# Performance work log

Hardware: AMD Instinct MI355X
Metric: run time of the kernel (lower is better)

Reference implementation:

```python
import jax, jax.numpy as jnp
import numpy as np

B = 16384          # batch
F = 26             # num sparse features
D = 13             # num dense features
V = 100000         # vocab per sparse feature
E = 16             # embedding size
HID = [400, 400, 400]
DNN_IN = F * E + D  # 429


def setup_inputs() -> dict:
    key = jax.random.key(0)
    ks = jax.random.split(key, 16)
    inp = {}
    inp["x_sparse"] = jax.random.randint(ks[0], (B, F), 0, V, dtype=jnp.int32)
    inp["x_dense"] = jax.random.uniform(ks[1], (B, D), dtype=jnp.float32)
    # embedding tables (stacked across features; all vocabs equal)
    inp["emb1"] = jax.random.normal(ks[2], (F, V, 1), dtype=jnp.float32) * 0.0001
    inp["emb2"] = jax.random.normal(ks[3], (F, V, E), dtype=jnp.float32) * 0.0001
    inp["w_dense"] = jax.random.normal(ks[4], (D, 1), dtype=jnp.float32) * 0.0001
    inp["bias"] = jnp.zeros((1,), dtype=jnp.float32)
    dims = [DNN_IN] + HID
    for i in range(3):
        inp[f"dnn_w{i}"] = jax.random.normal(ks[5 + i], (dims[i], dims[i + 1]), dtype=jnp.float32) * 0.02
        inp[f"dnn_b{i}"] = jnp.zeros((dims[i + 1],), dtype=jnp.float32)
    inp["final_w"] = jax.random.normal(ks[9], (HID[-1], 1), dtype=jnp.float32) * 0.02
    return inp


def reference(x_sparse, x_dense, emb1, emb2, w_dense, bias,
              dnn_w0, dnn_b0, dnn_w1, dnn_b1, dnn_w2, dnn_b2, final_w):
    f_idx = jnp.arange(F)[None, :]                      # [1, F]
    # FM linear: per-feature 1-d embedding lookup, summed over features
    e1 = emb1[f_idx, x_sparse, 0]                       # [B, F]
    linear_sparse = jnp.sum(e1, axis=-1, keepdims=True)  # [B, 1]
    linear_dense = x_dense @ w_dense                    # [B, 1]
    logit = linear_sparse + linear_dense
    # FM second order: square-of-sum minus sum-of-square
    fm = emb2[f_idx, x_sparse]                          # [B, F, E]
    s = jnp.sum(fm, axis=1)                             # [B, E]
    cross = 0.5 * jnp.sum(s * s - jnp.sum(fm * fm, axis=1), axis=-1, keepdims=True)  # [B, 1]
    logit = logit + cross
    # DNN
    h = jnp.concatenate([fm.reshape(x_sparse.shape[0], F * E), x_dense], axis=-1)  # [B, F*E+D]
    h = jax.nn.relu(h @ dnn_w0 + dnn_b0)
    h = jax.nn.relu(h @ dnn_w1 + dnn_b1)
    h = jax.nn.relu(h @ dnn_w2 + dnn_b2)
    logit = logit + h @ final_w                         # [B, 1]
    return jax.nn.sigmoid(logit + bias)
```

## Files before the change

### kernel.cpp

```cpp
#include <hip/hip_runtime.h>
#include <hip/hip_bf16.h>
#include <math.h>

#define BATCH 16384
#define NF 26
#define ND 13
#define VOC 100000
#define KP0 448
#define KP1 416
#define CS 112
#define NSL 4
#define NGB 4096
#define NPB 2240

typedef __bf16 bf16x8 __attribute__((ext_vector_type(8)));
typedef float f32x4 __attribute__((ext_vector_type(4)));
using bf16 = __hip_bfloat16;
typedef unsigned short u16;

__device__ __forceinline__ void gload_lds16(const void* g, void* l) {
  __builtin_amdgcn_global_load_lds(
      (const __attribute__((address_space(1))) void*)g,
      (__attribute__((address_space(3))) void*)l, 16, 0, 0);
}

__device__ __forceinline__ u16 f2bu(float v) {
  union { __hip_bfloat16 b; u16 u; } cv;
  cv.b = __float2bfloat16(v);
  return cv.u;
}

__global__ __launch_bounds__(256) void prep_gather_kernel(
    const float* __restrict__ w0, const float* __restrict__ w1,
    const float* __restrict__ w2, bf16* __restrict__ wt0,
    bf16* __restrict__ wt1, bf16* __restrict__ wt2,
    const int* __restrict__ xs, const float* __restrict__ xd,
    const float* __restrict__ emb1, const float* __restrict__ emb2,
    const float* __restrict__ wd, const float* __restrict__ biasp,
    bf16* __restrict__ h0, float* __restrict__ partial) {
  const int bid = blockIdx.x, tid = threadIdx.x;
  if (bid >= NGB) {
    const int pbid = bid - NGB;
    const float* W; bf16* Wt; int K, KP, idx;
    if (pbid < 784)       { W = w0; Wt = wt0; K = 429; KP = KP0; idx = pbid * 256 + tid; }
    else if (pbid < 1512) { W = w1; Wt = wt1; K = 400; KP = KP1; idx = (pbid - 784) * 256 + tid; }
    else                  { W = w2; Wt = wt2; K = 400; KP = KP1; idx = (pbid - 1512) * 256 + tid; }
    int k = idx % KP, n = idx / KP;
    float v = (k < K && n < 400) ? W[(size_t)k * 400 + n] : 0.f;
    Wt[idx] = __float2bfloat16(v);
    return;
  }
  const int p = bid;
  const int x8 = p & 7, qb = p >> 3;
  const int gl = (qb >> 5) * 256 + x8 * 32 + (qb & 31);
  const int w = tid >> 6, lane = tid & 63;
  const int b = gl * 4 + w;
  const int q = lane >> 2, sub = lane & 3;

  int xsl = 0;
  if (lane < NF) xsl = xs[b * NF + lane];
  float lin = 0.f;
  if (lane < NF) lin = emb1[(size_t)lane * VOC + xsl];
  if (lane < ND) lin += xd[b * ND + lane] * wd[lane];

  float4 sv = make_float4(0.f, 0.f, 0.f, 0.f);
  float sq = 0.f;
#pragma unroll
  for (int i = 0; i < 2; ++i) {
    int f = i * 16 + q;
    if (f < NF) {
      int idx = __shfl(xsl, f);
      float4 v = *((const float4*)(emb2 + ((size_t)f * VOC + idx) * 16) + sub);
      sv.x += v.x; sv.y += v.y; sv.z += v.z; sv.w += v.w;
      sq += v.x * v.x + v.y * v.y + v.z * v.z + v.w * v.w;
      ushort4 st;
      st.x = f2bu(v.x); st.y = f2bu(v.y); st.z = f2bu(v.z); st.w = f2bu(v.w);
      *(ushort4*)(h0 + (size_t)b * KP0 + f * 16 + sub * 4) = st;
    }
  }
  if (lane < 32) {
    float v = (lane < ND) ? xd[b * ND + lane] : 0.f;
    h0[(size_t)b * KP0 + 416 + lane] = __float2bfloat16(v);
  }
#pragma unroll
  for (int off = 4; off < 64; off <<= 1) {
    sv.x += __shfl_xor(sv.x, off);
    sv.y += __shfl_xor(sv.y, off);
    sv.z += __shfl_xor(sv.z, off);
    sv.w += __shfl_xor(sv.w, off);
  }
  float t = sv.x * sv.x + sv.y * sv.y + sv.z * sv.z + sv.w * sv.w;
#pragma unroll
  for (int off = 1; off < 64; off <<= 1) {
    t += __shfl_xor(t, off);
    sq += __shfl_xor(sq, off);
    lin += __shfl_xor(lin, off);
  }
  if (lane == 0)
    partial[b] = biasp[0] + lin + 0.5f * (t * 0.0625f - sq);
}

template <int NK, bool FINAL>
__global__ __launch_bounds__(256, 2) void gemm_kernel(
    const bf16* __restrict__ A, const bf16* __restrict__ Wt,
    const float* __restrict__ bias, bf16* __restrict__ outH,
    const float* __restrict__ fw, float* __restrict__ dotb) {
  constexpr int KP = NK * 32;
  constexpr int NKB = NK - 7;
  extern __shared__ __align__(16) char smem[];
  const int b = blockIdx.x, tid = threadIdx.x;
  const int w = tid >> 6, lane = tid & 63, r = lane & 15, g = lane >> 4;
  const int lane8 = b & 7, hi = b >> 3;
  const int s = hi & 3, mchunk = (hi >> 2) * 8 + lane8;
  const int row0 = mchunk * 128, col0 = s * CS;
  const char* wbase = (const char*)(Wt + (size_t)col0 * KP);

  auto stageP = [&](int kbase, int chunks) {
    for (int c0 = 0; c0 < chunks; c0 += 256) {
      int c = c0 + tid;
      if (c < chunks) {
        int kk = c / (CS * 4);
        int rm = c - kk * (CS * 4);
        int n = rm >> 2, j = rm & 3;
        int kc = j ^ ((n >> 1) & 3);
        gload_lds16(wbase + (size_t)n * (KP * 2) + (kbase + kk) * 64 + kc * 16,
                    smem + (c0 + w * 64) * 16);
      }
    }
  };

  const char* Ab = (const char*)(A + (size_t)(row0 + w * 32 + r) * KP) + g * 16;
  const size_t rtS = (size_t)16 * KP * 2;

  bf16x8 aA0[7], aA1[7];
#pragma unroll
  for (int k = 0; k < 7; ++k) {
    aA0[k] = *(const bf16x8*)(Ab + k * 64);
    aA1[k] = *(const bf16x8*)(Ab + k * 64 + rtS);
  }
  stageP(0, 7 * CS * 4);
  __syncthreads();

  bf16x8 aB0[NKB], aB1[NKB];
#pragma unroll
  for (int k = 0; k < NKB; ++k) {
    aB0[k] = *(const bf16x8*)(Ab + (7 + k) * 64);
    aB1[k] = *(const bf16x8*)(Ab + (7 + k) * 64 + rtS);
  }

  f32x4 acc[2][7];
#pragma unroll
  for (int rt = 0; rt < 2; ++rt)
#pragma unroll
    for (int ct = 0; ct < 7; ++ct) acc[rt][ct] = (f32x4){0.f, 0.f, 0.f, 0.f};

  const int swz = ((g ^ ((r >> 1) & 3)) << 4);
#pragma unroll
  for (int kk = 0; kk < 7; ++kk) {
    const char* sb = smem + kk * (CS * 64) + r * 64 + swz;
#pragma unroll
    for (int ct = 0; ct < 7; ++ct) {
      bf16x8 bfr = *(const bf16x8*)(sb + ct * 1024);
      acc[0][ct] = __builtin_amdgcn_mfma_f32_16x16x32_bf16(aA0[kk], bfr, acc[0][ct], 0, 0, 0);
      acc[1][ct] = __builtin_amdgcn_mfma_f32_16x16x32_bf16(aA1[kk], bfr, acc[1][ct], 0, 0, 0);
    }
  }
  __syncthreads();
  stageP(7, NKB * CS * 4);
  __syncthreads();
#pragma unroll
  for (int kk = 0; kk < NKB; ++kk) {
    const char* sb = smem + kk * (CS * 64) + r * 64 + swz;
#pragma unroll
    for (int ct = 0; ct < 7; ++ct) {
      bf16x8 bfr = *(const bf16x8*)(sb + ct * 1024);
      acc[0][ct] = __builtin_amdgcn_mfma_f32_16x16x32_bf16(aB0[kk], bfr, acc[0][ct], 0, 0, 0);
      acc[1][ct] = __builtin_amdgcn_mfma_f32_16x16x32_bf16(aB1[kk], bfr, acc[1][ct], 0, 0, 0);
    }
  }

  if (!FINAL) {
#pragma unroll
    for (int ct = 0; ct < 7; ++ct) {
      int col = col0 + ct * 16 + r;
      if (col < 400) {
        float bv = bias[col];
#pragma unroll
        for (int rt = 0; rt < 2; ++rt)
#pragma unroll
          for (int q = 0; q < 4; ++q) {
            float v = fmaxf(acc[rt][ct][q] + bv, 0.f);
            outH[(size_t)(row0 + w * 32 + rt * 16 + g * 4 + q) * KP1 + col] =
                __float2bfloat16(v);
          }
      }
    }
  } else {
    float pr[2][4] = {{0.f, 0.f, 0.f, 0.f}, {0.f, 0.f, 0.f, 0.f}};
#pragma unroll
    for (int ct = 0; ct < 7; ++ct) {
      int col = col0 + ct * 16 + r;
      if (col < 400) {
        float bv = bias[col], fv = fw[col];
#pragma unroll
        for (int rt = 0; rt < 2; ++rt)
#pragma unroll
          for (int q = 0; q < 4; ++q)
            pr[rt][q] += fmaxf(acc[rt][ct][q] + bv, 0.f) * fv;
      }
    }
#pragma unroll
    for (int rt = 0; rt < 2; ++rt)
#pragma unroll
      for (int q = 0; q < 4; ++q) {
        pr[rt][q] += __shfl_xor(pr[rt][q], 1);
        pr[rt][q] += __shfl_xor(pr[rt][q], 2);
        pr[rt][q] += __shfl_xor(pr[rt][q], 4);
        pr[rt][q] += __shfl_xor(pr[rt][q], 8);
      }
    if (r < 4) {
#pragma unroll
      for (int rt = 0; rt < 2; ++rt) {
        float v = (r == 0) ? pr[rt][0] : (r == 1) ? pr[rt][1]
                : (r == 2) ? pr[rt][2] : pr[rt][3];
        dotb[(size_t)s * BATCH + row0 + w * 32 + rt * 16 + g * 4 + r] = v;
      }
    }
  }
}

__global__ void finish_kernel(const float* __restrict__ partial,
                              const float* __restrict__ dotb,
                              float* __restrict__ out) {
  int i = blockIdx.x * 256 + threadIdx.x;
  if (i < BATCH) {
    float x = partial[i] + dotb[i] + dotb[BATCH + i] + dotb[2 * BATCH + i]
            + dotb[3 * BATCH + i];
    out[i] = 1.f / (1.f + expf(-x));
  }
}

extern "C" void kernel_launch(void* const* d_in, const int* in_sizes, int n_in,
                              void* d_out, int out_size, void* d_ws, size_t ws_size,
                              hipStream_t stream) {
  const int* xs = (const int*)d_in[0];
  const float* xd = (const float*)d_in[1];
  const float* emb1 = (const float*)d_in[2];
  const float* emb2 = (const float*)d_in[3];
  const float* wd = (const float*)d_in[4];
  const float* bias = (const float*)d_in[5];
  const float* w0 = (const float*)d_in[6];
  const float* b0 = (const float*)d_in[7];
  const float* w1 = (const float*)d_in[8];
  const float* b1 = (const float*)d_in[9];
  const float* w2 = (const float*)d_in[10];
  const float* b2 = (const float*)d_in[11];
  const float* fw = (const float*)d_in[12];
  float* out = (float*)d_out;

  char* ws = (char*)d_ws;
  float* partial = (float*)(ws + 0);
  float* dotb    = (float*)(ws + 65536);
  bf16* wt0 = (bf16*)(ws + 327680);
  bf16* wt1 = (bf16*)(ws + 729088);
  bf16* wt2 = (bf16*)(ws + 1101824);
  bf16* h0  = (bf16*)(ws + 1474560);
  bf16* h1  = (bf16*)(ws + 16154624);
  bf16* h2  = (bf16*)(ws + 29786112);

  constexpr int LDSB = 7 * CS * 64;
  hipFuncSetAttribute((const void*)gemm_kernel<14, false>,
                      hipFuncAttributeMaxDynamicSharedMemorySize, LDSB);
  hipFuncSetAttribute((const void*)gemm_kernel<13, false>,
                      hipFuncAttributeMaxDynamicSharedMemorySize, LDSB);
  hipFuncSetAttribute((const void*)gemm_kernel<13, true>,
                      hipFuncAttributeMaxDynamicSharedMemorySize, LDSB);

  prep_gather_kernel<<<NGB + NPB, 256, 0, stream>>>(
      w0, w1, w2, wt0, wt1, wt2, xs, xd, emb1, emb2, wd, bias, h0, partial);

  gemm_kernel<14, false><<<512, 256, LDSB, stream>>>(h0, wt0, b0, h1, nullptr, nullptr);
  gemm_kernel<13, false><<<512, 256, LDSB, stream>>>(h1, wt1, b1, h2, nullptr, nullptr);
  gemm_kernel<13, true><<<512, 256, LDSB, stream>>>(h2, wt2, b2, nullptr, fw, dotb);

  finish_kernel<<<64, 256, 0, stream>>>(partial, dotb, out);
}
```

Baseline: 64.95 us.

## Retile GEMM warps into 2x2 grid with 64-row by column-split tiles

Each block's four waves change from a 4x1 row split (32 rows by all 7 column tiles per wave) to a 2x2 grid (64 rows by 3 or 4 column tiles per wave). Each LDS B fragment now feeds four MFMAs instead of two, cutting LDS reads per MFMA, and the A fragments for the second K phase are loaded after the first phase to limit register pressure. The final layer writes 8 partial dot products instead of 4, so the finish kernel sums 8 and the workspace offsets shift. The cost is that the two column-group waves do unequal work (4 vs 3 tiles), and the A loads now issue later instead of overlapping the first phase.

Measured after the change: 84.24 us. +29.7%, slower.

```diff
diff --git a/kernel.cpp b/kernel.cpp
--- a/kernel.cpp
+++ b/kernel.cpp
@@ -110,6 +110,8 @@
   extern __shared__ __align__(16) char smem[];
   const int b = blockIdx.x, tid = threadIdx.x;
   const int w = tid >> 6, lane = tid & 63, r = lane & 15, g = lane >> 4;
+  const int rg = w >> 1, cgp = w & 1;
+  const int ntc = 4 - cgp, tb0 = cgp * 4;
   const int lane8 = b & 7, hi = b >> 3;
   const int s = hi & 3, mchunk = (hi >> 2) * 8 + lane8;
   const int row0 = mchunk * 128, col0 = s * CS;
@@ -129,88 +131,93 @@
     }
   };
 
-  const char* Ab = (const char*)(A + (size_t)(row0 + w * 32 + r) * KP) + g * 16;
+  const char* Ab = (const char*)(A + (size_t)(row0 + rg * 64 + r) * KP) + g * 16;
   const size_t rtS = (size_t)16 * KP * 2;
 
-  bf16x8 aA0[7], aA1[7];
-#pragma unroll
-  for (int k = 0; k < 7; ++k) {
-    aA0[k] = *(const bf16x8*)(Ab + k * 64);
-    aA1[k] = *(const bf16x8*)(Ab + k * 64 + rtS);
-  }
+  bf16x8 aA[4][7];
+#pragma unroll
+  for (int rt = 0; rt < 4; ++rt)
+#pragma unroll
+    for (int k = 0; k < 7; ++k)
+      aA[rt][k] = *(const bf16x8*)(Ab + k * 64 + rt * rtS);
   stageP(0, 7 * CS * 4);
   __syncthreads();
 
-  bf16x8 aB0[NKB], aB1[NKB];
-#pragma unroll
-  for (int k = 0; k < NKB; ++k) {
-    aB0[k] = *(const bf16x8*)(Ab + (7 + k) * 64);
-    aB1[k] = *(const bf16x8*)(Ab + (7 + k) * 64 + rtS);
-  }
-
-  f32x4 acc[2][7];
-#pragma unroll
-  for (int rt = 0; rt < 2; ++rt)
-#pragma unroll
-    for (int ct = 0; ct < 7; ++ct) acc[rt][ct] = (f32x4){0.f, 0.f, 0.f, 0.f};
+  f32x4 acc[4][4];
+#pragma unroll
+  for (int rt = 0; rt < 4; ++rt)
+#pragma unroll
+    for (int ct = 0; ct < 4; ++ct) acc[rt][ct] = (f32x4){0.f, 0.f, 0.f, 0.f};
 
   const int swz = ((g ^ ((r >> 1) & 3)) << 4);
 #pragma unroll
   for (int kk = 0; kk < 7; ++kk) {
     const char* sb = smem + kk * (CS * 64) + r * 64 + swz;
 #pragma unroll
-    for (int ct = 0; ct < 7; ++ct) {
-      bf16x8 bfr = *(const bf16x8*)(sb + ct * 1024);
-      acc[0][ct] = __builtin_amdgcn_mfma_f32_16x16x32_bf16(aA0[kk], bfr, acc[0][ct], 0, 0, 0);
-      acc[1][ct] = __builtin_amdgcn_mfma_f32_16x16x32_bf16(aA1[kk], bfr, acc[1][ct], 0, 0, 0);
-    }
+    for (int ct = 0; ct < 4; ++ct)
+      if (ct < ntc) {
+        bf16x8 bfr = *(const bf16x8*)(sb + (tb0 + ct) * 1024);
+#pragma unroll
+        for (int rt = 0; rt < 4; ++rt)
+          acc[rt][ct] = __builtin_amdgcn_mfma_f32_16x16x32_bf16(aA[rt][kk], bfr, acc[rt][ct], 0, 0, 0);
+      }
   }
   __syncthreads();
+#pragma unroll
+  for (int rt = 0; rt < 4; ++rt)
+#pragma unroll
+    for (int k = 0; k < NKB; ++k)
+      aA[rt][k] = *(const bf16x8*)(Ab + (7 + k) * 64 + rt * rtS);
   stageP(7, NKB * CS * 4);
   __syncthreads();
 #pragma unroll
   for (int kk = 0; kk < NKB; ++kk) {
     const char* sb = smem + kk * (CS * 64) + r * 64 + swz;
 #pragma unroll
-    for (int ct = 0; ct < 7; ++ct) {
-      bf16x8 bfr = *(const bf16x8*)(sb + ct * 1024);
-      acc[0][ct] = __builtin_amdgcn_mfma_f32_16x16x32_bf16(aB0[kk], bfr, acc[0][ct], 0, 0, 0);
-      acc[1][ct] = __builtin_amdgcn_mfma_f32_16x16x32_bf16(aB1[kk], bfr, acc[1][ct], 0, 0, 0);
-    }
+    for (int ct = 0; ct < 4; ++ct)
+      if (ct < ntc) {
+        bf16x8 bfr = *(const bf16x8*)(sb + (tb0 + ct) * 1024);
+#pragma unroll
+        for (int rt = 0; rt < 4; ++rt)
+          acc[rt][ct] = __builtin_amdgcn_mfma_f32_16x16x32_bf16(aA[rt][kk], bfr, acc[rt][ct], 0, 0, 0);
+      }
   }
 
   if (!FINAL) {
 #pragma unroll
-    for (int ct = 0; ct < 7; ++ct) {
-      int col = col0 + ct * 16 + r;
-      if (col < 400) {
-        float bv = bias[col];
-#pragma unroll
-        for (int rt = 0; rt < 2; ++rt)
-#pragma unroll
-          for (int q = 0; q < 4; ++q) {
-            float v = fmaxf(acc[rt][ct][q] + bv, 0.f);
-            outH[(size_t)(row0 + w * 32 + rt * 16 + g * 4 + q) * KP1 + col] =
-                __float2bfloat16(v);
-          }
-      }
-    }
+    for (int ct = 0; ct < 4; ++ct)
+      if (ct < ntc) {
+        int col = col0 + (tb0 + ct) * 16 + r;
+        if (col < 400) {
+          float bv = bias[col];
+#pragma unroll
+          for (int rt = 0; rt < 4; ++rt)
+#pragma unroll
+            for (int q = 0; q < 4; ++q) {
+              float v = fmaxf(acc[rt][ct][q] + bv, 0.f);
+              outH[(size_t)(row0 + rg * 64 + rt * 16 + g * 4 + q) * KP1 + col] =
+                  __float2bfloat16(v);
+            }
+        }
+      }
   } else {
-    float pr[2][4] = {{0.f, 0.f, 0.f, 0.f}, {0.f, 0.f, 0.f, 0.f}};
-#pragma unroll
-    for (int ct = 0; ct < 7; ++ct) {
-      int col = col0 + ct * 16 + r;
-      if (col < 400) {
-        float bv = bias[col], fv = fw[col];
-#pragma unroll
-        for (int rt = 0; rt < 2; ++rt)
-#pragma unroll
-          for (int q = 0; q < 4; ++q)
-            pr[rt][q] += fmaxf(acc[rt][ct][q] + bv, 0.f) * fv;
-      }
-    }
-#pragma unroll
-    for (int rt = 0; rt < 2; ++rt)
+    float pr[4][4] = {{0.f,0.f,0.f,0.f},{0.f,0.f,0.f,0.f},
+                      {0.f,0.f,0.f,0.f},{0.f,0.f,0.f,0.f}};
+#pragma unroll
+    for (int ct = 0; ct < 4; ++ct)
+      if (ct < ntc) {
+        int col = col0 + (tb0 + ct) * 16 + r;
+        if (col < 400) {
+          float bv = bias[col], fv = fw[col];
+#pragma unroll
+          for (int rt = 0; rt < 4; ++rt)
+#pragma unroll
+            for (int q = 0; q < 4; ++q)
+              pr[rt][q] += fmaxf(acc[rt][ct][q] + bv, 0.f) * fv;
+        }
+      }
+#pragma unroll
+    for (int rt = 0; rt < 4; ++rt)
 #pragma unroll
       for (int q = 0; q < 4; ++q) {
         pr[rt][q] += __shfl_xor(pr[rt][q], 1);
@@ -220,10 +227,10 @@
       }
     if (r < 4) {
 #pragma unroll
-      for (int rt = 0; rt < 2; ++rt) {
+      for (int rt = 0; rt < 4; ++rt) {
         float v = (r == 0) ? pr[rt][0] : (r == 1) ? pr[rt][1]
                 : (r == 2) ? pr[rt][2] : pr[rt][3];
-        dotb[(size_t)s * BATCH + row0 + w * 32 + rt * 16 + g * 4 + r] = v;
+        dotb[(size_t)(s * 2 + cgp) * BATCH + row0 + rg * 64 + rt * 16 + g * 4 + r] = v;
       }
     }
   }
@@ -234,8 +241,9 @@
                               float* __restrict__ out) {
   int i = blockIdx.x * 256 + threadIdx.x;
   if (i < BATCH) {
-    float x = partial[i] + dotb[i] + dotb[BATCH + i] + dotb[2 * BATCH + i]
-            + dotb[3 * BATCH + i];
+    float x = partial[i];
+#pragma unroll
+    for (int j = 0; j < 8; ++j) x += dotb[(size_t)j * BATCH + i];
     out[i] = 1.f / (1.f + expf(-x));
   }
 }
@@ -261,12 +269,12 @@
   char* ws = (char*)d_ws;
   float* partial = (float*)(ws + 0);
   float* dotb    = (float*)(ws + 65536);
-  bf16* wt0 = (bf16*)(ws + 327680);
-  bf16* wt1 = (bf16*)(ws + 729088);
-  bf16* wt2 = (bf16*)(ws + 1101824);
-  bf16* h0  = (bf16*)(ws + 1474560);
-  bf16* h1  = (bf16*)(ws + 16154624);
-  bf16* h2  = (bf16*)(ws + 29786112);
+  bf16* wt0 = (bf16*)(ws + 589824);
+  bf16* wt1 = (bf16*)(ws + 991232);
+  bf16* wt2 = (bf16*)(ws + 1363968);
+  bf16* h0  = (bf16*)(ws + 1736704);
+  bf16* h1  = (bf16*)(ws + 16416768);
+  bf16* h2  = (bf16*)(ws + 30048256);
 
   constexpr int LDSB = 7 * CS * 64;
   hipFuncSetAttribute((const void*)gemm_kernel<14, false>,
```

## Double-buffer weight staging in LDS across three K phases in GEMM

Applied to the files above, without the earlier changes.

Splits the GEMM K loop into three phases over two LDS buffers. Each phase's weight slab is loaded asynchronously into one buffer while MFMAs consume the other, and the A-fragment register loads for the next phase are issued ahead of the current compute. This is meant to hide the global-to-LDS staging latency that used to sit behind a barrier before the second K half. In exchange, LDS per block grows from about 49 KB to 70 KB, which reduces headroom for two resident blocks per CU, and the kernel now has an extra phase and barrier.

Result: slower. 67.04 us (+3.2%).

```diff
diff --git a/kernel.cpp b/kernel.cpp
--- a/kernel.cpp
+++ b/kernel.cpp
@@ -12,6 +12,7 @@
 #define NSL 4
 #define NGB 4096
 #define NPB 2240
+#define PHB (5 * CS * 64)
 
 typedef __bf16 bf16x8 __attribute__((ext_vector_type(8)));
 typedef float f32x4 __attribute__((ext_vector_type(4)));
@@ -106,8 +107,10 @@
     const float* __restrict__ bias, bf16* __restrict__ outH,
     const float* __restrict__ fw, float* __restrict__ dotb) {
   constexpr int KP = NK * 32;
-  constexpr int NKB = NK - 7;
+  constexpr int P0 = 5, P1 = (NK == 14) ? 5 : 4, P2 = 4;
   extern __shared__ __align__(16) char smem[];
+  char* buf0 = smem;
+  char* buf1 = smem + PHB;
   const int b = blockIdx.x, tid = threadIdx.x;
   const int w = tid >> 6, lane = tid & 63, r = lane & 15, g = lane >> 4;
   const int lane8 = b & 7, hi = b >> 3;
@@ -115,7 +118,7 @@
   const int row0 = mchunk * 128, col0 = s * CS;
   const char* wbase = (const char*)(Wt + (size_t)col0 * KP);
 
-  auto stageP = [&](int kbase, int chunks) {
+  auto stageP = [&](int kbase, int chunks, char* dst) {
     for (int c0 = 0; c0 < chunks; c0 += 256) {
       int c = c0 + tid;
       if (c < chunks) {
@@ -124,40 +127,40 @@
         int n = rm >> 2, j = rm & 3;
         int kc = j ^ ((n >> 1) & 3);
         gload_lds16(wbase + (size_t)n * (KP * 2) + (kbase + kk) * 64 + kc * 16,
-                    smem + (c0 + w * 64) * 16);
+                    dst + (c0 + w * 64) * 16);
       }
     }
   };
 
   const char* Ab = (const char*)(A + (size_t)(row0 + w * 32 + r) * KP) + g * 16;
   const size_t rtS = (size_t)16 * KP * 2;
-
-  bf16x8 aA0[7], aA1[7];
-#pragma unroll
-  for (int k = 0; k < 7; ++k) {
+  const int swz = ((g ^ ((r >> 1) & 3)) << 4);
+
+  f32x4 acc[2][7];
+#pragma unroll
+  for (int rt = 0; rt < 2; ++rt)
+#pragma unroll
+    for (int ct = 0; ct < 7; ++ct) acc[rt][ct] = (f32x4){0.f, 0.f, 0.f, 0.f};
+
+  bf16x8 aA0[P0], aA1[P0];
+#pragma unroll
+  for (int k = 0; k < P0; ++k) {
     aA0[k] = *(const bf16x8*)(Ab + k * 64);
     aA1[k] = *(const bf16x8*)(Ab + k * 64 + rtS);
   }
-  stageP(0, 7 * CS * 4);
+  stageP(0, P0 * CS * 4, buf0);
   __syncthreads();
 
-  bf16x8 aB0[NKB], aB1[NKB];
-#pragma unroll
-  for (int k = 0; k < NKB; ++k) {
-    aB0[k] = *(const bf16x8*)(Ab + (7 + k) * 64);
-    aB1[k] = *(const bf16x8*)(Ab + (7 + k) * 64 + rtS);
-  }
-
-  f32x4 acc[2][7];
-#pragma unroll
-  for (int rt = 0; rt < 2; ++rt)
-#pragma unroll
-    for (int ct = 0; ct < 7; ++ct) acc[rt][ct] = (f32x4){0.f, 0.f, 0.f, 0.f};
-
-  const int swz = ((g ^ ((r >> 1) & 3)) << 4);
-#pragma unroll
-  for (int kk = 0; kk < 7; ++kk) {
-    const char* sb = smem + kk * (CS * 64) + r * 64 + swz;
+  bf16x8 aB0[P1], aB1[P1];
+#pragma unroll
+  for (int k = 0; k < P1; ++k) {
+    aB0[k] = *(const bf16x8*)(Ab + (P0 + k) * 64);
+    aB1[k] = *(const bf16x8*)(Ab + (P0 + k) * 64 + rtS);
+  }
+  stageP(P0, P1 * CS * 4, buf1);
+#pragma unroll
+  for (int kk = 0; kk < P0; ++kk) {
+    const char* sb = buf0 + kk * (CS * 64) + r * 64 + swz;
 #pragma unroll
     for (int ct = 0; ct < 7; ++ct) {
       bf16x8 bfr = *(const bf16x8*)(sb + ct * 1024);
@@ -166,16 +169,34 @@
     }
   }
   __syncthreads();
-  stageP(7, NKB * CS * 4);
-  __syncthreads();
-#pragma unroll
-  for (int kk = 0; kk < NKB; ++kk) {
-    const char* sb = smem + kk * (CS * 64) + r * 64 + swz;
+
+  bf16x8 aC0[P2], aC1[P2];
+#pragma unroll
+  for (int k = 0; k < P2; ++k) {
+    aC0[k] = *(const bf16x8*)(Ab + (P0 + P1 + k) * 64);
+    aC1[k] = *(const bf16x8*)(Ab + (P0 + P1 + k) * 64 + rtS);
+  }
+  stageP(P0 + P1, P2 * CS * 4, buf0);
+#pragma unroll
+  for (int kk = 0; kk < P1; ++kk) {
+    const char* sb = buf1 + kk * (CS * 64) + r * 64 + swz;
 #pragma unroll
     for (int ct = 0; ct < 7; ++ct) {
       bf16x8 bfr = *(const bf16x8*)(sb + ct * 1024);
       acc[0][ct] = __builtin_amdgcn_mfma_f32_16x16x32_bf16(aB0[kk], bfr, acc[0][ct], 0, 0, 0);
       acc[1][ct] = __builtin_amdgcn_mfma_f32_16x16x32_bf16(aB1[kk], bfr, acc[1][ct], 0, 0, 0);
+    }
+  }
+  __syncthreads();
+
+#pragma unroll
+  for (int kk = 0; kk < P2; ++kk) {
+    const char* sb = buf0 + kk * (CS * 64) + r * 64 + swz;
+#pragma unroll
+    for (int ct = 0; ct < 7; ++ct) {
+      bf16x8 bfr = *(const bf16x8*)(sb + ct * 1024);
+      acc[0][ct] = __builtin_amdgcn_mfma_f32_16x16x32_bf16(aC0[kk], bfr, acc[0][ct], 0, 0, 0);
+      acc[1][ct] = __builtin_amdgcn_mfma_f32_16x16x32_bf16(aC1[kk], bfr, acc[1][ct], 0, 0, 0);
     }
   }
 
@@ -268,7 +289,7 @@
   bf16* h1  = (bf16*)(ws + 16154624);
   bf16* h2  = (bf16*)(ws + 29786112);
 
-  constexpr int LDSB = 7 * CS * 64;
+  constexpr int LDSB = 2 * PHB;
   hipFuncSetAttribute((const void*)gemm_kernel<14, false>,
                       hipFuncAttributeMaxDynamicSharedMemorySize, LDSB);
   hipFuncSetAttribute((const void*)gemm_kernel<13, false>,
```
